# Kernel optimization log

Measured on AMD Instinct MI355X. Metric: run time of the kernel, lower is better.

Reference implementation:

```python
import jax, jax.numpy as jnp
import numpy as np

DIM = 512
HEADS = 8
DIM_HEAD = 64
HIDDEN = HEADS * DIM_HEAD  # 512
SCALE = DIM_HEAD ** -0.5
EPS = 1e-12  # F.normalize default eps


def rms_norm(x, g):
    # F.normalize over channel dim (dim=1), then * g * sqrt(C)
    c = x.shape[1]
    norm = jnp.sqrt(jnp.sum(x * x, axis=1, keepdims=True))
    return x / jnp.maximum(norm, EPS) * g * (c ** 0.5)


def setup_inputs() -> dict:
    key = jax.random.key(0)
    ks = jax.random.split(key, 6)
    b, h, w = 16, 64, 64
    x = jax.random.normal(ks[0], (b, DIM, h, w), dtype=jnp.float32)
    g1 = jnp.ones((1, DIM, 1, 1), dtype=jnp.float32)
    # 1x1 conv weights stored as (out_ch, in_ch)
    Wqkv = jax.random.normal(ks[1], (HIDDEN * 3, DIM), dtype=jnp.float32) * (DIM ** -0.5)
    Wout = jax.random.normal(ks[2], (DIM, HIDDEN), dtype=jnp.float32) * (HIDDEN ** -0.5)
    bout = jax.random.normal(ks[3], (DIM,), dtype=jnp.float32) * 0.01
    g2 = jnp.ones((1, DIM, 1, 1), dtype=jnp.float32)
    return {"x": x, "g1": g1, "Wqkv": Wqkv, "Wout": Wout, "bout": bout, "g2": g2}


def reference(x, g1, Wqkv, Wout, bout, g2):
    b, c, h, w = x.shape
    n = h * w
    xn = rms_norm(x, g1)
    # 1x1 conv == channel matmul
    qkv = jnp.einsum('oc,bchw->bohw', Wqkv, xn)  # (b, 3*hidden, h, w)
    qkv = qkv.reshape(b, 3, HEADS, DIM_HEAD, n)
    q, k, v = qkv[:, 0], qkv[:, 1], qkv[:, 2]  # (b, heads, d, n)
    q = jax.nn.softmax(q, axis=-2) * SCALE      # softmax over feature dim
    k = jax.nn.softmax(k, axis=-1)               # softmax over spatial dim
    context = jnp.einsum('bhdn,bhen->bhde', k, v)  # (b,h,d,e) small
    out = jnp.einsum('bhde,bhdn->bhen', context, q)  # (b,h,e,n)
    out = out.reshape(b, HIDDEN, h, w)
    out = jnp.einsum('oc,bchw->bohw', Wout, out) + bout[None, :, None, None]
    return rms_norm(out, g2)
```

## Files before the change

kernel.cpp:

```cpp
#include <hip/hip_runtime.h>
#include <hip/hip_bf16.h>
#include <math.h>

#define B_ 16
#define C_ 512
#define N_ 4096
#define NCOL (B_ * N_)

typedef short bf16x8 __attribute__((ext_vector_type(8)));
typedef ushort ushort8_t __attribute__((ext_vector_type(8)));
typedef float f32x4 __attribute__((ext_vector_type(4)));

__device__ __forceinline__ ushort f2bf(float f) {
    unsigned u = __float_as_uint(f);
    unsigned r = (u + 0x7FFFu + ((u >> 16) & 1u)) >> 16;
    return (ushort)r;
}
__device__ __forceinline__ float bf2f(ushort u) {
    return __uint_as_float((unsigned)u << 16);
}
__device__ __forceinline__ void gload_lds16(const void* g, void* l) {
    __builtin_amdgcn_global_load_lds(
        (const __attribute__((address_space(1))) unsigned int*)g,
        (__attribute__((address_space(3))) unsigned int*)l, 16, 0, 0);
}

__global__ __launch_bounds__(256) void wprep2_k(const float* __restrict__ Wqkv,
                                                const float* __restrict__ g1,
                                                const float* __restrict__ Wout,
                                                ushort* __restrict__ Wqkvb,
                                                ushort* __restrict__ Woutb)
{
    int i = blockIdx.x * 256 + threadIdx.x;
    if (i < 196608) {
        float4 wv = reinterpret_cast<const float4*>(Wqkv)[i];
        const float4 gv = *reinterpret_cast<const float4*>(g1 + ((i * 4) & 511));
        ushort4 u;
        u.x = f2bf(wv.x * gv.x); u.y = f2bf(wv.y * gv.y);
        u.z = f2bf(wv.z * gv.z); u.w = f2bf(wv.w * gv.w);
        reinterpret_cast<ushort4*>(Wqkvb)[i] = u;
    } else {
        int j = i - 196608;
        float4 wv = reinterpret_cast<const float4*>(Wout)[j];
        ushort4 u;
        u.x = f2bf(wv.x); u.y = f2bf(wv.y); u.z = f2bf(wv.z); u.w = f2bf(wv.w);
        reinterpret_cast<ushort4*>(Woutb)[j] = u;
    }
}

__global__ __launch_bounds__(256) void transpose_k(const float* __restrict__ X,
                                                   ushort* __restrict__ Xt,
                                                   float* __restrict__ rs1)
{
    __shared__ float t[2][64][68];
    __shared__ float sr[16][64];
    const int b = blockIdx.y, n0 = blockIdx.x * 64;
    const int tid = threadIdx.x;
    const int tg = tid >> 4, tl = tid & 15;
    float sq[4] = {0.f, 0.f, 0.f, 0.f};
    for (int chunk = 0; chunk < 8; ++chunk) {
        const int buf = chunk & 1;
        const float* xp = X + ((size_t)b * C_ + chunk * 64) * N_ + n0;
        #pragma unroll
        for (int j = 0; j < 4; ++j) {
            int c = tg + j * 16;
            float4 v = *reinterpret_cast<const float4*>(xp + (size_t)c * N_ + tl * 4);
            *reinterpret_cast<float4*>(&t[buf][c][tl * 4]) = v;
            sq[0] += v.x * v.x; sq[1] += v.y * v.y;
            sq[2] += v.z * v.z; sq[3] += v.w * v.w;
        }
        __syncthreads();
        #pragma unroll
        for (int i = 0; i < 4; ++i) {
            int nl = tg + i * 16, cl = tl * 4;
            ushort4 u;
            u.x = f2bf(t[buf][cl + 0][nl]);
            u.y = f2bf(t[buf][cl + 1][nl]);
            u.z = f2bf(t[buf][cl + 2][nl]);
            u.w = f2bf(t[buf][cl + 3][nl]);
            *reinterpret_cast<ushort4*>(
                Xt + ((size_t)b * N_ + n0 + nl) * 512 + chunk * 64 + cl) = u;
        }
    }
    #pragma unroll
    for (int j = 0; j < 4; ++j) sr[tg][tl * 4 + j] = sq[j];
    __syncthreads();
    if (tid < 64) {
        float s = 0.f;
        #pragma unroll
        for (int g = 0; g < 16; ++g) s += sr[g][tid];
        rs1[(size_t)b * N_ + n0 + tid] = 22.627416998f / fmaxf(sqrtf(s), 1e-12f);
    }
}

template <bool SWAP>
__global__ __launch_bounds__(512, 2)
void mfma_gemm(const ushort* __restrict__ A, const ushort* __restrict__ Bt,
               const float* __restrict__ rs1,
               ushort* __restrict__ qT2, ushort* __restrict__ kd,
               ushort* __restrict__ vd, int m_off)
{
    __shared__ __align__(16) char lds[2][2][32768];
    const int b  = blockIdx.z;
    const int n0 = blockIdx.x * 256;
    const int m0 = m_off + blockIdx.y * 256;
    const int tid = threadIdx.x;
    const int w = tid >> 6, l = tid & 63;
    const int wm = w >> 2, wn = w & 3;
    const int lq = l >> 4, lr = l & 15;
    const ushort* Bb = Bt + (size_t)b * N_ * 512;

    f32x4 acc[8][4];
    #pragma unroll
    for (int i = 0; i < 8; ++i)
        #pragma unroll
        for (int j = 0; j < 4; ++j)
            #pragma unroll
            for (int r = 0; r < 4; ++r) acc[i][j][r] = 0.f;

#define STAGE_STEP(t, i)                                                      \
    do {                                                                      \
        const int kb_ = (t) * 128;                                            \
        const int idx_ = (i) * 512 + tid;                                     \
        const int r_ = idx_ >> 3;                                             \
        const int ch_ = (idx_ & 7) ^ (r_ & 7);                                \
        gload_lds16((const char*)A + (size_t)(m0 + r_) * 1024 + kb_ + ch_ * 16,\
                    &lds[(t) & 1][0][idx_ * 16]);                             \
        gload_lds16((const char*)Bb + (size_t)(n0 + r_) * 1024 + kb_ + ch_ * 16,\
                    &lds[(t) & 1][1][idx_ * 16]);                             \
    } while (0)

    #pragma unroll
    for (int i = 0; i < 4; ++i) STAGE_STEP(0, i);

    bf16x8 bfr[4];
    #pragma unroll 2
    for (int t = 0; t < 8; ++t) {
        const char* As = lds[t & 1][0];
        const char* Bs = lds[t & 1][1];
        #pragma unroll
        for (int ph = 0; ph < 4; ++ph) {
            const int kk = ph >> 1, mg = ph & 1;
            bf16x8 af[4];
            if (ph != 0) {
                #pragma unroll
                for (int m2 = 0; m2 < 4; ++m2) {
                    int ra = wm * 128 + (mg * 4 + m2) * 16 + lr;
                    int ch = (kk * 4 + lq) ^ (ra & 7);
                    af[m2] = *(const bf16x8*)(As + ra * 128 + ch * 16);
                }
                if (mg == 0) {
                    #pragma unroll
                    for (int nf = 0; nf < 4; ++nf) {
                        int rb = wn * 64 + nf * 16 + lr;
                        int ch = (kk * 4 + lq) ^ (rb & 7);
                        bfr[nf] = *(const bf16x8*)(Bs + rb * 128 + ch * 16);
                    }
                }
            }
            if (t < 7) STAGE_STEP(t + 1, ph);
            if (ph == 0) {
                if (t < 7) { asm volatile("s_waitcnt vmcnt(2)" ::: "memory"); }
                else       { asm volatile("s_waitcnt vmcnt(0)" ::: "memory"); }
            }
            __builtin_amdgcn_s_barrier();
            if (ph == 0) {
                #pragma unroll
                for (int m2 = 0; m2 < 4; ++m2) {
                    int ra = wm * 128 + m2 * 16 + lr;
                    int ch = lq ^ (ra & 7);
                    af[m2] = *(const bf16x8*)(As + ra * 128 + ch * 16);
                }
                #pragma unroll
                for (int nf = 0; nf < 4; ++nf) {
                    int rb = wn * 64 + nf * 16 + lr;
                    int ch = lq ^ (rb & 7);
                    bfr[nf] = *(const bf16x8*)(Bs + rb * 128 + ch * 16);
                }
            }
            asm volatile("s_waitcnt lgkmcnt(0)" ::: "memory");
            __builtin_amdgcn_sched_barrier(0);
            __builtin_amdgcn_s_setprio(1);
            #pragma unroll
            for (int m2 = 0; m2 < 4; ++m2)
                #pragma unroll
                for (int nf = 0; nf < 4; ++nf) {
                    if constexpr (SWAP)
                        acc[mg * 4 + m2][nf] = __builtin_amdgcn_mfma_f32_16x16x32_bf16(
                            bfr[nf], af[m2], acc[mg * 4 + m2][nf], 0, 0, 0);
                    else
                        acc[mg * 4 + m2][nf] = __builtin_amdgcn_mfma_f32_16x16x32_bf16(
                            af[m2], bfr[nf], acc[mg * 4 + m2][nf], 0, 0, 0);
                }
            __builtin_amdgcn_s_setprio(0);
            __builtin_amdgcn_s_barrier();
        }
    }
#undef STAGE_STEP

    const int nbase = n0 + wn * 64;
    if constexpr (!SWAP) {
        const int mloc = (m0 & 511) + wm * 128;
        #pragma unroll
        for (int hg = 0; hg < 2; ++hg) {
            const int head = (mloc >> 6) + hg;
            #pragma unroll
            for (int nf = 0; nf < 4; ++nf) {
                const int n = nbase + nf * 16 + lr;
                const float sc = rs1[(size_t)b * N_ + n];
                float v[4][4];
                float mx = -1e30f;
                #pragma unroll
                for (int m2 = 0; m2 < 4; ++m2)
                    #pragma unroll
                    for (int r = 0; r < 4; ++r) {
                        v[m2][r] = acc[hg * 4 + m2][nf][r] * sc;
                        mx = fmaxf(mx, v[m2][r]);
                    }
                mx = fmaxf(mx, __shfl_xor(mx, 16));
                mx = fmaxf(mx, __shfl_xor(mx, 32));
                float s = 0.f;
                #pragma unroll
                for (int m2 = 0; m2 < 4; ++m2)
                    #pragma unroll
                    for (int r = 0; r < 4; ++r) {
                        v[m2][r] = __expf(v[m2][r] - mx);
                        s += v[m2][r];
                    }
                s += __shfl_xor(s, 16);
                s += __shfl_xor(s, 32);
                const float r8 = 0.125f / s;
                ushort* qp = qT2 + ((size_t)b * N_ + n) * 512 + head * 64;
                #pragma unroll
                for (int m2 = 0; m2 < 4; ++m2) {
                    ushort4 u;
                    u.x = f2bf(v[m2][0] * r8);
                    u.y = f2bf(v[m2][1] * r8);
                    u.z = f2bf(v[m2][2] * r8);
                    u.w = f2bf(v[m2][3] * r8);
                    *reinterpret_cast<ushort4*>(qp + m2 * 16 + lq * 4) = u;
                }
            }
        }
    } else {
        const int part = m0 >> 9;
        const int mloc = (m0 & 511) + wm * 128;
        ushort* dst = (part == 1) ? kd : vd;
        float4 sc4[4];
        #pragma unroll
        for (int nf = 0; nf < 4; ++nf)
            sc4[nf] = *reinterpret_cast<const float4*>(
                rs1 + (size_t)b * N_ + nbase + nf * 16 + lq * 4);
        #pragma unroll
        for (int mf = 0; mf < 8; ++mf) {
            char* reg = &lds[0][0][w * 4096 + (mf & 1) * 2048];
            #pragma unroll
            for (int nf = 0; nf < 4; ++nf) {
                ushort4 u;
                u.x = f2bf(acc[mf][nf][0] * sc4[nf].x);
                u.y = f2bf(acc[mf][nf][1] * sc4[nf].y);
                u.z = f2bf(acc[mf][nf][2] * sc4[nf].z);
                u.w = f2bf(acc[mf][nf][3] * sc4[nf].w);
                const int col2 = (nf * 16 + lq * 4) * 2;
                *reinterpret_cast<ushort4*>(
                    reg + lr * 128 + (col2 ^ ((lr & 7) << 4))) = u;
            }
            asm volatile("s_waitcnt lgkmcnt(0)" ::: "memory");
            const int rho = l >> 3;
            const int nc = (l & 7) * 16;
            bf16x8 v0 = *(const bf16x8*)(reg + rho * 128 + (nc ^ ((rho & 7) << 4)));
            bf16x8 v1 = *(const bf16x8*)(reg + (rho + 8) * 128 + (nc ^ ((rho & 7) << 4)));
            const size_t ro = (size_t)b * 512 + mloc + mf * 16;
            *(bf16x8*)(dst + (ro + rho) * N_ + nbase + (l & 7) * 8) = v0;
            *(bf16x8*)(dst + (ro + rho + 8) * N_ + nbase + (l & 7) * 8) = v1;
        }
    }
}

__global__ __launch_bounds__(256) void rowstat_k(const ushort* __restrict__ kk,
                                                 float* __restrict__ rowm,
                                                 float* __restrict__ rowr)
{
    const int row = blockIdx.x * 4 + (threadIdx.x >> 6);
    const int lane = threadIdx.x & 63;
    const ushort* p = kk + (size_t)row * N_;
    float vals[64];
    #pragma unroll
    for (int j = 0; j < 8; ++j) {
        ushort8_t u = *reinterpret_cast<const ushort8_t*>(p + lane * 8 + j * 512);
        #pragma unroll
        for (int t = 0; t < 8; ++t) vals[j * 8 + t] = bf2f(u[t]);
    }
    float mx = -1e30f;
    #pragma unroll
    for (int i = 0; i < 64; ++i) mx = fmaxf(mx, vals[i]);
    #pragma unroll
    for (int o = 32; o >= 1; o >>= 1) mx = fmaxf(mx, __shfl_xor(mx, o));
    float s = 0.f;
    #pragma unroll
    for (int i = 0; i < 64; ++i) s += __expf(vals[i] - mx);
    #pragma unroll
    for (int o = 32; o >= 1; o >>= 1) s += __shfl_xor(s, o);
    if (lane == 0) { rowm[row] = mx; rowr[row] = 1.f / s; }
}

__global__ __launch_bounds__(256) void ctx_k(const ushort* __restrict__ kk,
                                             const ushort* __restrict__ vv,
                                             const float* __restrict__ rowm,
                                             const float* __restrict__ rowr,
                                             float* __restrict__ ctxp)
{
    const int bh = blockIdx.x, chunk = blockIdx.y;
    const ushort* kp = kk + (size_t)bh * 64 * N_;
    const ushort* vp = vv + (size_t)bh * 64 * N_;
    __shared__ __align__(16) ushort kx[64 * 128];
    __shared__ __align__(16) ushort vx[64 * 128];
    __shared__ float rm[64];
    const int tid = threadIdx.x;
    const int w = tid >> 6, l = tid & 63;
    const int lq = l >> 4, lr = l & 15;
    const int we = w >> 1, wd = w & 1;
    if (tid < 64) rm[tid] = rowm[(size_t)bh * 64 + tid];
    __syncthreads();

    f32x4 acc[2][2];
    #pragma unroll
    for (int i = 0; i < 2; ++i)
        #pragma unroll
        for (int j = 0; j < 2; ++j)
            #pragma unroll
            for (int r = 0; r < 4; ++r) acc[i][j][r] = 0.f;

    for (int s = 0; s < 8; ++s) {
        const int n0 = chunk * 1024 + s * 128;
        #pragma unroll
        for (int i = 0; i < 4; ++i) {
            int idx = i * 256 + tid;
            int row = idx >> 4;
            int ch  = (idx & 15) ^ (row & 15);
            gload_lds16((const char*)(vp + (size_t)row * N_ + n0 + ch * 8),
                        (char*)vx + idx * 16);
        }
        #pragma unroll
        for (int i = 0; i < 4; ++i) {
            int idx = i * 256 + tid;
            int row = idx >> 4;
            int ch  = idx & 15;
            ushort8_t u = *reinterpret_cast<const ushort8_t*>(
                kp + (size_t)row * N_ + n0 + ch * 8);
            float m_ = rm[row];
            ushort8_t o;
            #pragma unroll
            for (int t = 0; t < 8; ++t) o[t] = f2bf(__expf(bf2f(u[t]) - m_));
            *(ushort8_t*)((char*)kx + (row * 16 + (ch ^ (row & 15))) * 16) = o;
        }
        __syncthreads();
        #pragma unroll
        for (int k2 = 0; k2 < 4; ++k2) {
            bf16x8 af[2], bfr[2];
            #pragma unroll
            for (int i = 0; i < 2; ++i) {
                int re = we * 32 + i * 16 + lr;
                int cha = (k2 * 4 + lq) ^ (re & 15);
                af[i] = *(const bf16x8*)((const char*)vx + (re * 16 + cha) * 16);
                int rd = wd * 32 + i * 16 + lr;
                int chb = (k2 * 4 + lq) ^ (rd & 15);
                bfr[i] = *(const bf16x8*)((const char*)kx + (rd * 16 + chb) * 16);
            }
            #pragma unroll
            for (int i = 0; i < 2; ++i)
                #pragma unroll
                for (int j = 0; j < 2; ++j)
                    acc[i][j] = __builtin_amdgcn_mfma_f32_16x16x32_bf16(
                        af[i], bfr[j], acc[i][j], 0, 0, 0);
        }
        __syncthreads();
    }
    float* cbase = ctxp + ((size_t)bh * 4 + chunk) * 4096;
    #pragma unroll
    for (int j = 0; j < 2; ++j) {
        const int d = wd * 32 + j * 16 + lr;
        const float rr = rowr[(size_t)bh * 64 + d];
        #pragma unroll
        for (int i = 0; i < 2; ++i) {
            const int e0 = we * 32 + i * 16 + lq * 4;
            float4 wv;
            wv.x = acc[i][j][0] * rr;
            wv.y = acc[i][j][1] * rr;
            wv.z = acc[i][j][2] * rr;
            wv.w = acc[i][j][3] * rr;
            *reinterpret_cast<float4*>(cbase + (size_t)d * 64 + e0) = wv;
        }
    }
}

__global__ __launch_bounds__(256) void wcbuild_k(const ushort* __restrict__ Wb,
                                                 const float* __restrict__ ctxp,
                                                 ushort* __restrict__ Wc)
{
    const int oh = blockIdx.x, h = blockIdx.y, b = blockIdx.z;
    const int bh = b * 8 + h;
    __shared__ __align__(16) ushort ws[256 * 64];
    __shared__ __align__(16) ushort cs[64 * 64];
    const int tid = threadIdx.x;
    const int w = tid >> 6, l = tid & 63;
    const int lq = l >> 4, lr = l & 15;

    #pragma unroll
    for (int i = 0; i < 8; ++i) {
        int idx = i * 256 + tid;
        int row = idx >> 3;
        int ch = (idx & 7) ^ (row & 7);
        gload_lds16(Wb + (size_t)(oh * 256 + row) * 512 + h * 64 + ch * 8,
                    (char*)ws + idx * 16);
    }
    {
        const float* cp = ctxp + (size_t)bh * 4 * 4096;
        const int d = tid >> 2, eb = (tid & 3) * 16;
        float vs[16];
        #pragma unroll
        for (int t4 = 0; t4 < 4; ++t4) {
            float4 a0 = *(const float4*)(cp + d * 64 + eb + t4 * 4);
            float4 a1 = *(const float4*)(cp + 4096 + d * 64 + eb + t4 * 4);
            float4 a2 = *(const float4*)(cp + 8192 + d * 64 + eb + t4 * 4);
            float4 a3 = *(const float4*)(cp + 12288 + d * 64 + eb + t4 * 4);
            vs[t4 * 4 + 0] = a0.x + a1.x + a2.x + a3.x;
            vs[t4 * 4 + 1] = a0.y + a1.y + a2.y + a3.y;
            vs[t4 * 4 + 2] = a0.z + a1.z + a2.z + a3.z;
            vs[t4 * 4 + 3] = a0.w + a1.w + a2.w + a3.w;
        }
        ushort8_t o0, o1;
        #pragma unroll
        for (int t = 0; t < 8; ++t) { o0[t] = f2bf(vs[t]); o1[t] = f2bf(vs[8 + t]); }
        const int c0 = (eb >> 3) ^ (d & 7);
        const int c1 = ((eb >> 3) + 1) ^ (d & 7);
        *(ushort8_t*)((char*)cs + (d * 8 + c0) * 16) = o0;
        *(ushort8_t*)((char*)cs + (d * 8 + c1) * 16) = o1;
    }
    __syncthreads();

    f32x4 acc[4][4];
    #pragma unroll
    for (int i = 0; i < 4; ++i)
        #pragma unroll
        for (int j = 0; j < 4; ++j)
            #pragma unroll
            for (int r = 0; r < 4; ++r) acc[i][j][r] = 0.f;

    #pragma unroll
    for (int kk = 0; kk < 2; ++kk) {
        bf16x8 af[4], bfr[4];
        #pragma unroll
        for (int mf = 0; mf < 4; ++mf) {
            int ra = w * 64 + mf * 16 + lr;
            int ch = (kk * 4 + lq) ^ (ra & 7);
            af[mf] = *(const bf16x8*)((const char*)ws + (ra * 8 + ch) * 16);
        }
        #pragma unroll
        for (int nf = 0; nf < 4; ++nf) {
            int rd = nf * 16 + lr;
            int ch = (kk * 4 + lq) ^ (rd & 7);
            bfr[nf] = *(const bf16x8*)((const char*)cs + (rd * 8 + ch) * 16);
        }
        #pragma unroll
        for (int mf = 0; mf < 4; ++mf)
            #pragma unroll
            for (int nf = 0; nf < 4; ++nf)
                acc[mf][nf] = __builtin_amdgcn_mfma_f32_16x16x32_bf16(
                    af[mf], bfr[nf], acc[mf][nf], 0, 0, 0);
    }

    ushort* wp = Wc + (size_t)b * 262144 + h * 64;
    #pragma unroll
    for (int mf = 0; mf < 4; ++mf)
        #pragma unroll
        for (int r = 0; r < 4; ++r) {
            const int o = oh * 256 + w * 64 + mf * 16 + lq * 4 + r;
            #pragma unroll
            for (int nf = 0; nf < 4; ++nf)
                wp[(size_t)o * 512 + nf * 16 + lr] = f2bf(acc[mf][nf][r]);
        }
}

__global__ __launch_bounds__(512, 2)
void gemm2_k(const ushort* __restrict__ Wc,
             const ushort* __restrict__ Bt,
             const float* __restrict__ bias,
             const float* __restrict__ g2,
             float* __restrict__ outp)
{
    __shared__ __align__(16) ushort As[512 * 64];
    __shared__ __align__(16) ushort Bs[128 * 64];
    const int b  = blockIdx.y;
    const int n0 = blockIdx.x * 128;
    const int tid = threadIdx.x;
    const int w = tid >> 6, l = tid & 63;
    const int lq = l >> 4, lr = l & 15;
    const ushort* A  = Wc + (size_t)b * 262144;
    const ushort* Bb = Bt + (size_t)b * N_ * 512;

    f32x4 acc[4][8];
    #pragma unroll
    for (int i = 0; i < 4; ++i)
        #pragma unroll
        for (int j = 0; j < 8; ++j)
            #pragma unroll
            for (int r = 0; r < 4; ++r) acc[i][j][r] = 0.f;

    for (int k0 = 0; k0 < 512; k0 += 64) {
        #pragma unroll
        for (int i = 0; i < 8; ++i) {
            int base = i * 512 + w * 64;
            int idx = base + l;
            int r = idx >> 3, ch = (idx & 7) ^ (r & 7);
            gload_lds16((const char*)A + (size_t)r * 1024 + k0 * 2 + ch * 16,
                        (char*)As + (size_t)base * 16);
        }
        #pragma unroll
        for (int i = 0; i < 2; ++i) {
            int base = i * 512 + w * 64;
            int idx = base + l;
            int r = idx >> 3, ch = (idx & 7) ^ (r & 7);
            gload_lds16((const char*)Bb + (size_t)(n0 + r) * 1024 + k0 * 2 + ch * 16,
                        (char*)Bs + (size_t)base * 16);
        }
        __syncthreads();
        #pragma unroll
        for (int kk = 0; kk < 2; ++kk) {
            bf16x8 af[4], bfv[8];
            #pragma unroll
            for (int mf = 0; mf < 4; ++mf) {
                int ra = w * 64 + mf * 16 + lr;
                int ch = (kk * 4 + lq) ^ (ra & 7);
                af[mf] = *(const bf16x8*)((const char*)As + ra * 128 + ch * 16);
            }
            #pragma unroll
            for (int nf = 0; nf < 8; ++nf) {
                int rb = nf * 16 + lr;
                int ch = (kk * 4 + lq) ^ (rb & 7);
                bfv[nf] = *(const bf16x8*)((const char*)Bs + rb * 128 + ch * 16);
            }
            #pragma unroll
            for (int mf = 0; mf < 4; ++mf)
                #pragma unroll
                for (int nf = 0; nf < 8; ++nf)
                    acc[mf][nf] = __builtin_amdgcn_mfma_f32_16x16x32_bf16(
                        af[mf], bfv[nf], acc[mf][nf], 0, 0, 0);
        }
        __syncthreads();
    }

    float4 bv[4], g2v[4];
    #pragma unroll
    for (int mf = 0; mf < 4; ++mf) {
        bv[mf]  = *reinterpret_cast<const float4*>(bias + w * 64 + mf * 16 + lq * 4);
        g2v[mf] = *reinterpret_cast<const float4*>(g2   + w * 64 + mf * 16 + lq * 4);
    }
    float csq[8] = {};
    #pragma unroll
    for (int mf = 0; mf < 4; ++mf)
        #pragma unroll
        for (int nf = 0; nf < 8; ++nf)
            #pragma unroll
            for (int r = 0; r < 4; ++r) {
                float wv = acc[mf][nf][r] + ((const float*)&bv[mf])[r];
                acc[mf][nf][r] = wv;
                csq[nf] += wv * wv;
            }
    #pragma unroll
    for (int nf = 0; nf < 8; ++nf) {
        csq[nf] += __shfl_xor(csq[nf], 16);
        csq[nf] += __shfl_xor(csq[nf], 32);
    }
    float* red  = (float*)As;
    float* rs2s = red + 1024;
    if (lq == 0) {
        #pragma unroll
        for (int nf = 0; nf < 8; ++nf)
            red[w * 128 + nf * 16 + lr] = csq[nf];
    }
    __syncthreads();
    if (tid < 128) {
        float s = 0.f;
        #pragma unroll
        for (int j = 0; j < 8; ++j) s += red[j * 128 + tid];
        rs2s[tid] = 22.627416998f / fmaxf(sqrtf(s), 1e-12f);
    }
    __syncthreads();
    #pragma unroll
    for (int nf = 0; nf < 8; ++nf) {
        const float rsv = rs2s[nf * 16 + lr];
        const int n = n0 + nf * 16 + lr;
        #pragma unroll
        for (int mf = 0; mf < 4; ++mf) {
            const int o = w * 64 + mf * 16 + lq * 4;
            float* p = outp + ((size_t)b * 512 + o) * N_ + n;
            #pragma unroll
            for (int r = 0; r < 4; ++r)
                p[(size_t)r * N_] = acc[mf][nf][r] * rsv * ((const float*)&g2v[mf])[r];
        }
    }
}

extern "C" void kernel_launch(void* const* d_in, const int* in_sizes, int n_in,
                              void* d_out, int out_size, void* d_ws, size_t ws_size,
                              hipStream_t stream)
{
    const float* x    = (const float*)d_in[0];
    const float* g1   = (const float*)d_in[1];
    const float* Wqkv = (const float*)d_in[2];
    const float* Wout = (const float*)d_in[3];
    const float* bout = (const float*)d_in[4];
    const float* g2   = (const float*)d_in[5];
    float* out = (float*)d_out;

    char* wsb = (char*)d_ws;
    ushort* qbuf  = (ushort*)wsb;
    ushort* kbuf  = (ushort*)(wsb + ((size_t)64 << 20));
    ushort* vbuf  = (ushort*)(wsb + ((size_t)128 << 20));
    ushort* Xt    = (ushort*)(wsb + ((size_t)192 << 20));
    float*  ctxp  = (float*)Xt;
    float*  rowm  = (float*)(wsb + ((size_t)200 << 20));
    float*  rowr  = rowm + 8192;
    ushort* Wcb   = (ushort*)(wsb + ((size_t)201 << 20));
    char*   tail  = wsb + ((size_t)256 << 20);
    ushort* Wqkvb = (ushort*)tail;
    ushort* Woutb = (ushort*)(tail + (size_t)1536 * 512 * 2);
    float*  rs1   = (float*)(tail + (size_t)1536 * 512 * 2 + (size_t)512 * 512 * 2);

    wprep2_k<<<1024, 256, 0, stream>>>(Wqkv, g1, Wout, Wqkvb, Woutb);
    transpose_k<<<dim3(64, 16), 256, 0, stream>>>(x, Xt, rs1);
    mfma_gemm<false><<<dim3(16, 2, B_), 512, 0, stream>>>(Wqkvb, Xt, rs1,
                                                          qbuf, kbuf, vbuf, 0);
    mfma_gemm<true><<<dim3(16, 4, B_), 512, 0, stream>>>(Wqkvb, Xt, rs1,
                                                         qbuf, kbuf, vbuf, 512);
    rowstat_k<<<2048, 256, 0, stream>>>(kbuf, rowm, rowr);
    ctx_k<<<dim3(B_ * 8, 4), 256, 0, stream>>>(kbuf, vbuf, rowm, rowr, ctxp);
    wcbuild_k<<<dim3(2, 8, B_), 256, 0, stream>>>(Woutb, ctxp, Wcb);
    gemm2_k<<<dim3(32, B_), 512, 0, stream>>>(Wcb, qbuf, bout, g2, out);
}
```

Baseline: 320.7 us.

## Merge QKV GEMM launches and store K/V directly without LDS transpose

Replaces the two templated GEMM launches (Q path and swapped K/V path) with one launch covering all six row blocks, branching on the part index at runtime. The K/V epilogue no longer swaps MFMA operands and restages through LDS for coalesced 16-byte stores. It now writes scaled bf16 values one element at a time straight to global memory. This removes a launch and the LDS round trip, but the K/V stores become 2-byte scattered writes with poor coalescing, which could raise memory traffic cost considerably.

Result: faster. 305.1 us (median of 2 runs) (-4.9%).

```diff
diff --git a/kernel.cpp b/kernel.cpp
--- a/kernel.cpp
+++ b/kernel.cpp
@@ -93,17 +93,16 @@
     }
 }
 
-template <bool SWAP>
 __global__ __launch_bounds__(512, 2)
 void mfma_gemm(const ushort* __restrict__ A, const ushort* __restrict__ Bt,
                const float* __restrict__ rs1,
                ushort* __restrict__ qT2, ushort* __restrict__ kd,
-               ushort* __restrict__ vd, int m_off)
+               ushort* __restrict__ vd)
 {
     __shared__ __align__(16) char lds[2][2][32768];
     const int b  = blockIdx.z;
     const int n0 = blockIdx.x * 256;
-    const int m0 = m_off + blockIdx.y * 256;
+    const int m0 = blockIdx.y * 256;
     const int tid = threadIdx.x;
     const int w = tid >> 6, l = tid & 63;
     const int wm = w >> 2, wn = w & 3;
@@ -184,23 +183,19 @@
             #pragma unroll
             for (int m2 = 0; m2 < 4; ++m2)
                 #pragma unroll
-                for (int nf = 0; nf < 4; ++nf) {
-                    if constexpr (SWAP)
-                        acc[mg * 4 + m2][nf] = __builtin_amdgcn_mfma_f32_16x16x32_bf16(
-                            bfr[nf], af[m2], acc[mg * 4 + m2][nf], 0, 0, 0);
-                    else
-                        acc[mg * 4 + m2][nf] = __builtin_amdgcn_mfma_f32_16x16x32_bf16(
-                            af[m2], bfr[nf], acc[mg * 4 + m2][nf], 0, 0, 0);
-                }
+                for (int nf = 0; nf < 4; ++nf)
+                    acc[mg * 4 + m2][nf] = __builtin_amdgcn_mfma_f32_16x16x32_bf16(
+                        af[m2], bfr[nf], acc[mg * 4 + m2][nf], 0, 0, 0);
             __builtin_amdgcn_s_setprio(0);
             __builtin_amdgcn_s_barrier();
         }
     }
 #undef STAGE_STEP
 
+    const int part = m0 >> 9;
+    const int mloc = (m0 & 511) + wm * 128;
     const int nbase = n0 + wn * 64;
-    if constexpr (!SWAP) {
-        const int mloc = (m0 & 511) + wm * 128;
+    if (part == 0) {
         #pragma unroll
         for (int hg = 0; hg < 2; ++hg) {
             const int head = (mloc >> 6) + hg;
@@ -243,36 +238,19 @@
             }
         }
     } else {
-        const int part = m0 >> 9;
-        const int mloc = (m0 & 511) + wm * 128;
         ushort* dst = (part == 1) ? kd : vd;
-        float4 sc4[4];
-        #pragma unroll
-        for (int nf = 0; nf < 4; ++nf)
-            sc4[nf] = *reinterpret_cast<const float4*>(
-                rs1 + (size_t)b * N_ + nbase + nf * 16 + lq * 4);
-        #pragma unroll
-        for (int mf = 0; mf < 8; ++mf) {
-            char* reg = &lds[0][0][w * 4096 + (mf & 1) * 2048];
-            #pragma unroll
-            for (int nf = 0; nf < 4; ++nf) {
-                ushort4 u;
-                u.x = f2bf(acc[mf][nf][0] * sc4[nf].x);
-                u.y = f2bf(acc[mf][nf][1] * sc4[nf].y);
-                u.z = f2bf(acc[mf][nf][2] * sc4[nf].z);
-                u.w = f2bf(acc[mf][nf][3] * sc4[nf].w);
-                const int col2 = (nf * 16 + lq * 4) * 2;
-                *reinterpret_cast<ushort4*>(
-                    reg + lr * 128 + (col2 ^ ((lr & 7) << 4))) = u;
-            }
-            asm volatile("s_waitcnt lgkmcnt(0)" ::: "memory");
-            const int rho = l >> 3;
-            const int nc = (l & 7) * 16;
-            bf16x8 v0 = *(const bf16x8*)(reg + rho * 128 + (nc ^ ((rho & 7) << 4)));
-            bf16x8 v1 = *(const bf16x8*)(reg + (rho + 8) * 128 + (nc ^ ((rho & 7) << 4)));
-            const size_t ro = (size_t)b * 512 + mloc + mf * 16;
-            *(bf16x8*)(dst + (ro + rho) * N_ + nbase + (l & 7) * 8) = v0;
-            *(bf16x8*)(dst + (ro + rho + 8) * N_ + nbase + (l & 7) * 8) = v1;
+        #pragma unroll
+        for (int nf = 0; nf < 4; ++nf) {
+            const int n = nbase + nf * 16 + lr;
+            const float sc = rs1[(size_t)b * N_ + n];
+            #pragma unroll
+            for (int mf = 0; mf < 8; ++mf) {
+                const int o = mloc + mf * 16 + lq * 4;
+                #pragma unroll
+                for (int r = 0; r < 4; ++r)
+                    dst[((size_t)b * 512 + o + r) * N_ + n] =
+                        f2bf(acc[mf][nf][r] * sc);
+            }
         }
     }
 }
@@ -630,10 +608,8 @@
 
     wprep2_k<<<1024, 256, 0, stream>>>(Wqkv, g1, Wout, Wqkvb, Woutb);
     transpose_k<<<dim3(64, 16), 256, 0, stream>>>(x, Xt, rs1);
-    mfma_gemm<false><<<dim3(16, 2, B_), 512, 0, stream>>>(Wqkvb, Xt, rs1,
-                                                          qbuf, kbuf, vbuf, 0);
-    mfma_gemm<true><<<dim3(16, 4, B_), 512, 0, stream>>>(Wqkvb, Xt, rs1,
-                                                         qbuf, kbuf, vbuf, 512);
+    mfma_gemm<<<dim3(16, 6, B_), 512, 0, stream>>>(Wqkvb, Xt, rs1,
+                                                   qbuf, kbuf, vbuf);
     rowstat_k<<<2048, 256, 0, stream>>>(kbuf, rowm, rowr);
     ctx_k<<<dim3(B_ * 8, 4), 256, 0, stream>>>(kbuf, vbuf, rowm, rowr, ctxp);
     wcbuild_k<<<dim3(2, 8, B_), 256, 0, stream>>>(Woutb, ctxp, Wcb);
```
